# Kernel tuning notes

Hardware: AMD Instinct MI355X
Metric: run time of the kernel (lower is better)

Reference implementation:

```python
import jax, jax.numpy as jnp
import numpy as np

B, D, H, W = 1, 4, 48, 48
C, NH = 256, 8
HD = C // NH
KD, KH, KW = 3, 5, 5
KVOL = KD * KH * KW
SCALE = HD ** -0.5


def _nbhd(L, k):
    """Neighborhood start indices (clamped to stay in-bounds, natten semantics)
    and relative-position-bias indices for one axis."""
    i = jnp.arange(L)
    start = jnp.clip(i - k // 2, 0, L - k)            # [L]
    idx = start[:, None] + jnp.arange(k)[None, :]     # [L,k] absolute neighbor index
    rel = idx - i[:, None] + (k - 1)                  # [L,k] rpb index in [0, 2k-2]
    return idx, rel


def setup_inputs() -> dict:
    key = jax.random.key(0)
    ks = jax.random.split(key, 5)
    s = 0.02
    return {
        "x": jax.random.normal(ks[0], (B, D, H, W, C), jnp.float32),
        "w_qkv": jax.random.normal(ks[1], (C, 3 * C), jnp.float32) * s,
        "b_qkv": jnp.zeros((3 * C,), jnp.float32),
        "rpb": jax.random.normal(ks[2], (NH, 2 * KD - 1, 2 * KH - 1, 2 * KW - 1), jnp.float32) * s,
        "w_proj": jax.random.normal(ks[3], (C, C), jnp.float32) * s,
        "b_proj": jnp.zeros((C,), jnp.float32),
    }


def _nat3d(q, k, v, rpb):
    # q,k,v: [B,NH,D,H,W,HD]; q already scaled
    idxD, relD = _nbhd(D, KD)
    idxH, relH = _nbhd(H, KH)
    idxW, relW = _nbhd(W, KW)
    iD = idxD[:, None, None, :, None, None]
    iH = idxH[None, :, None, None, :, None]
    iW = idxW[None, None, :, None, None, :]
    gk = k[:, :, iD, iH, iW]   # [B,NH,D,H,W,KD,KH,KW,HD]
    gv = v[:, :, iD, iH, iW]
    bias = rpb[:, relD[:, None, None, :, None, None],
                  relH[None, :, None, None, :, None],
                  relW[None, None, :, None, None, :]]  # [NH,D,H,W,KD,KH,KW]
    scores = jnp.einsum("bndyxc,bndyxtuvc->bndyxtuv", q, gk) + bias[None]
    flat = scores.reshape(*scores.shape[:5], KVOL)
    attn = jax.nn.softmax(flat, axis=-1).reshape(scores.shape)
    return jnp.einsum("bndyxtuv,bndyxtuvc->bndyxc", attn, gv)


def reference(x, w_qkv, b_qkv, rpb, w_proj, b_proj):
    qkv = (x @ w_qkv + b_qkv).reshape(B, D, H, W, 3, NH, HD)
    qkv = jnp.transpose(qkv, (4, 0, 5, 1, 2, 3, 6))  # [3,B,NH,D,H,W,HD]
    q, k, v = qkv[0] * SCALE, qkv[1], qkv[2]
    out = _nat3d(q, k, v, rpb)                       # [B,NH,D,H,W,HD]
    out = jnp.transpose(out, (0, 2, 3, 4, 1, 5)).reshape(B, D, H, W, C)
    return out @ w_proj + b_proj
```

## Files before the change

### kernel.cpp

```cpp
#include <hip/hip_runtime.h>

#define QK_SCALE 0.17677669529663687f
#define TOKENS 9216

typedef __attribute__((ext_vector_type(8))) __bf16 bf16x8;
typedef __attribute__((ext_vector_type(8))) unsigned short us8;
typedef __attribute__((ext_vector_type(4))) float f32x4;

static __device__ __forceinline__ unsigned short f2bf(float x) {
    unsigned int u = __float_as_uint(x);
    return (unsigned short)((u + 0x7FFFu + ((u >> 16) & 1u)) >> 16);
}
static __device__ __forceinline__ float bf2f(unsigned short u) {
    return __uint_as_float(((unsigned int)u) << 16);
}
static __device__ __forceinline__ bf16x8 ld_bf8(const unsigned short* p) {
    us8 u = *reinterpret_cast<const us8*>(p);
    return __builtin_bit_cast(bf16x8, u);
}

__global__ __launch_bounds__(256) void conv_prep(
    const float* __restrict__ x, const float* __restrict__ wqkv, const float* __restrict__ wproj,
    const float* __restrict__ rpb,
    unsigned short* __restrict__ xb, unsigned short* __restrict__ wqT,
    unsigned short* __restrict__ wpT, unsigned short* __restrict__ biasT)
{
    int b = blockIdx.x, t = threadIdx.x;
    if (b < 2304) {
        int idx = (b * 256 + t) * 4;
        float4 v = *reinterpret_cast<const float4*>(x + idx);
        ushort4 o;
        o.x = f2bf(v.x); o.y = f2bf(v.y); o.z = f2bf(v.z); o.w = f2bf(v.w);
        *reinterpret_cast<ushort4*>(xb + idx) = o;
    } else if (b < 3072) {
        int e = (b - 2304) * 256 + t;
        int n = e >> 8, k = e & 255;
        wqT[n * 256 + k] = f2bf(wqkv[k * 768 + n]);
    } else if (b < 3328) {
        int e = (b - 3072) * 256 + t;
        int n = e >> 8, k = e & 255;
        wpT[n * 256 + k] = f2bf(wproj[k * 256 + n]);
    } else {
        const int bid = b - 3328;
        const int cls = bid >> 3, h = bid & 7;
        const int d  = cls / 9;
        const int r  = cls % 9;
        const int yc = r / 3, xc = r % 3;
        const int by = (yc == 0) ? 0 : ((yc == 1) ? 5 : 11);
        const int bx = (xc == 0) ? 0 : ((xc == 1) ? 5 : 11);
        const int y0 = by * 4, x0 = bx * 4;
        const int base_d = min(max(d - 1, 0), 1);
        const int base_h = min(max(y0 - 2, 0), 40);
        const int base_w = min(max(x0 - 2, 0), 40);
        const int relD = base_d - d + 2;
        unsigned short* dst = biasT + (size_t)bid * 3072;
        for (int idx = t; idx < 3072; idx += 256) {
            int tok = idx / 192;
            int rem = idx - tok * 192;
            int w = rem / 96; rem -= w * 96;
            int g = rem / 24;
            int j = rem - g * 24;
            int i = j >> 2, rg = j & 3;
            int cand = w * 96 + i * 16 + g * 4 + rg;
            int y = y0 + (tok >> 2), xx = x0 + (tok & 3);
            int sh = min(max(y - 2, 0), 43), sw = min(max(xx - 2, 0), 43);
            int ld = cand >> 6, lh = (cand >> 3) & 7, lw = cand & 7;
            int t0 = lh - (sh - base_h), t1 = lw - (sw - base_w);
            bool valid = ((unsigned)t0 < 5u) && ((unsigned)t1 < 5u);
            unsigned short v = 0xFF80;
            if (valid) {
                int bi = (relD + ld) * 81 + (lh - (y - base_h) + 4) * 9 + (lw - (xx - base_w) + 4);
                v = f2bf(rpb[h * 405 + bi]);
            }
            dst[idx] = v;
        }
    }
}

template<int MF, int NF, int MODE>
__global__ __launch_bounds__(256) void gemm_mfma(
    const unsigned short* __restrict__ A, const unsigned short* __restrict__ BT,
    const float* __restrict__ bias,
    unsigned short* __restrict__ oq, unsigned short* __restrict__ ok,
    unsigned short* __restrict__ ov, float* __restrict__ of)
{
    const int tid = threadIdx.x;
    const int wid = tid >> 6, lane = tid & 63;
    const int wm = wid >> 1, wn = wid & 1;
    const int n15 = lane & 15, g = lane >> 4;
    const int m0 = blockIdx.y * (MF * 32) + wm * (MF * 16);
    const int n0 = blockIdx.x * (NF * 32) + wn * (NF * 16);

    f32x4 acc[MF][NF];
    #pragma unroll
    for (int i = 0; i < MF; i++)
        #pragma unroll
        for (int j = 0; j < NF; j++)
            acc[i][j] = f32x4{0.f, 0.f, 0.f, 0.f};

    #pragma unroll
    for (int ks = 0; ks < 8; ++ks) {
        bf16x8 a[MF], b[NF];
        #pragma unroll
        for (int mt = 0; mt < MF; ++mt)
            a[mt] = ld_bf8(A + (size_t)(m0 + mt * 16 + n15) * 256 + ks * 32 + g * 8);
        #pragma unroll
        for (int nt = 0; nt < NF; ++nt)
            b[nt] = ld_bf8(BT + (size_t)(n0 + nt * 16 + n15) * 256 + ks * 32 + g * 8);
        #pragma unroll
        for (int mt = 0; mt < MF; ++mt)
            #pragma unroll
            for (int nt = 0; nt < NF; ++nt)
                acc[mt][nt] = __builtin_amdgcn_mfma_f32_16x16x32_bf16(b[nt], a[mt], acc[mt][nt], 0, 0, 0);
    }

    #pragma unroll
    for (int mt = 0; mt < MF; ++mt) {
        #pragma unroll
        for (int nt = 0; nt < NF; ++nt) {
            int tok = m0 + mt * 16 + n15;
            int nb  = n0 + nt * 16 + g * 4;
            float4 bv4 = *reinterpret_cast<const float4*>(bias + nb);
            float v0 = acc[mt][nt][0] + bv4.x;
            float v1 = acc[mt][nt][1] + bv4.y;
            float v2 = acc[mt][nt][2] + bv4.z;
            float v3 = acc[mt][nt][3] + bv4.w;
            if (MODE == 0) {
                int part = nb >> 8, c = nb & 255, hh = c >> 5, ch = c & 31;
                unsigned short* dst = (part == 0) ? oq : ((part == 1) ? ok : ov);
                if (part == 0) { v0 *= QK_SCALE; v1 *= QK_SCALE; v2 *= QK_SCALE; v3 *= QK_SCALE; }
                ushort4 o;
                o.x = f2bf(v0); o.y = f2bf(v1); o.z = f2bf(v2); o.w = f2bf(v3);
                *reinterpret_cast<ushort4*>(dst + ((size_t)hh * TOKENS + tok) * 32 + ch) = o;
            } else {
                float4 o = make_float4(v0, v1, v2, v3);
                *reinterpret_cast<float4*>(of + (size_t)tok * 256 + nb) = o;
            }
        }
    }
}

__global__ __launch_bounds__(128) void nat_attn_mfma(
    const unsigned short* __restrict__ qws, const unsigned short* __restrict__ kws,
    const unsigned short* __restrict__ vws, const unsigned short* __restrict__ biasT,
    unsigned short* __restrict__ aout)
{
    __shared__ unsigned short VT[32 * 200];
    __shared__ unsigned short Pl[16 * 200];
    __shared__ float red[2][16];

    const int tid = threadIdx.x;
    const int w = tid >> 6, lane = tid & 63;
    const int n15 = lane & 15, g = lane >> 4;

    int b = blockIdx.x;
    const int h = b & 7; b >>= 3;
    const int bx = b % 12; b /= 12;
    const int by = b % 12;
    const int d  = b / 12;
    const int y0 = by * 4, x0 = bx * 4;
    const int base_d = min(max(d - 1, 0), 1);
    const int base_h = min(max(y0 - 2, 0), 40);
    const int base_w = min(max(x0 - 2, 0), 40);

    const int yc = (by == 0) ? 0 : ((by == 11) ? 2 : 1);
    const int xc = (bx == 0) ? 0 : ((bx == 11) ? 2 : 1);
    const unsigned short* bT = biasT + (size_t)(((d * 9 + yc * 3 + xc) * 8 + h)) * 3072;

    const size_t hoff = (size_t)h * TOKENS * 32;
    const unsigned short* kb = kws + hoff;
    const unsigned short* vb = vws + hoff;
    const unsigned short* qb = qws + hoff;

    for (int id = tid; id < 768; id += 128) {
        int cand = id % 192, chg = id / 192;
        int ld = cand >> 6, lh = (cand >> 3) & 7, lw = cand & 7;
        int gt = (base_d + ld) * 2304 + (base_h + lh) * 48 + (base_w + lw);
        us8 u = *reinterpret_cast<const us8*>(vb + (size_t)gt * 32 + chg * 8);
        #pragma unroll
        for (int e = 0; e < 8; e++) VT[(chg * 8 + e) * 200 + cand] = u[e];
    }

    us8 bl[3];
    {
        const unsigned short* bp = bT + (size_t)(((n15 * 2 + w) * 4 + g) * 24);
        bl[0] = *reinterpret_cast<const us8*>(bp);
        bl[1] = *reinterpret_cast<const us8*>(bp + 8);
        bl[2] = *reinterpret_cast<const us8*>(bp + 16);
    }

    const int gtq = d * 2304 + (y0 + (n15 >> 2)) * 48 + (x0 + (n15 & 3));
    bf16x8 qf = ld_bf8(qb + (size_t)gtq * 32 + g * 8);

    f32x4 sf[6];
    #pragma unroll
    for (int i = 0; i < 6; ++i) {
        int cand = (w * 6 + i) * 16 + n15;
        int ld = cand >> 6, lh = (cand >> 3) & 7, lw = cand & 7;
        int gtc = (base_d + ld) * 2304 + (base_h + lh) * 48 + (base_w + lw);
        bf16x8 kf = ld_bf8(kb + (size_t)gtc * 32 + g * 8);
        sf[i] = __builtin_amdgcn_mfma_f32_16x16x32_bf16(kf, qf, f32x4{0.f, 0.f, 0.f, 0.f}, 0, 0, 0);
    }

    float s24 = 0.f;
    uint2 pq[6];
    #pragma unroll
    for (int i = 0; i < 6; ++i) {
        int j = i * 4;
        float e0 = __expf(sf[i][0] + bf2f(bl[(j + 0) >> 3][(j + 0) & 7]));
        float e1 = __expf(sf[i][1] + bf2f(bl[(j + 1) >> 3][(j + 1) & 7]));
        float e2 = __expf(sf[i][2] + bf2f(bl[(j + 2) >> 3][(j + 2) & 7]));
        float e3 = __expf(sf[i][3] + bf2f(bl[(j + 3) >> 3][(j + 3) & 7]));
        s24 += (e0 + e1) + (e2 + e3);
        pq[i].x = (__float_as_uint(e1) & 0xFFFF0000u) | (__float_as_uint(e0) >> 16);
        pq[i].y = (__float_as_uint(e3) & 0xFFFF0000u) | (__float_as_uint(e2) >> 16);
    }
    s24 += __shfl_xor(s24, 16);
    s24 += __shfl_xor(s24, 32);
    if (g == 0) red[w][n15] = s24;

    #pragma unroll
    for (int i = 0; i < 6; ++i)
        *reinterpret_cast<uint2*>(&Pl[n15 * 200 + w * 96 + i * 16 + g * 4]) = pq[i];
    __syncthreads();

    f32x4 oacc = f32x4{0.f, 0.f, 0.f, 0.f};
    #pragma unroll
    for (int ks = 0; ks < 6; ++ks) {
        bf16x8 vf = ld_bf8(&VT[(w * 16 + n15) * 200 + ks * 32 + g * 8]);
        bf16x8 pa = ld_bf8(&Pl[n15 * 200 + ks * 32 + g * 8]);
        oacc = __builtin_amdgcn_mfma_f32_16x16x32_bf16(vf, pa, oacc, 0, 0, 0);
    }
    {
        float inv = 1.f / (red[0][n15] + red[1][n15]);
        int gtr = d * 2304 + (y0 + (n15 >> 2)) * 48 + (x0 + (n15 & 3));
        ushort4 o;
        o.x = f2bf(oacc[0] * inv);
        o.y = f2bf(oacc[1] * inv);
        o.z = f2bf(oacc[2] * inv);
        o.w = f2bf(oacc[3] * inv);
        *reinterpret_cast<ushort4*>(aout + (size_t)gtr * 256 + h * 32 + w * 16 + g * 4) = o;
    }
}

extern "C" void kernel_launch(void* const* d_in, const int* in_sizes, int n_in,
                              void* d_out, int out_size, void* d_ws, size_t ws_size,
                              hipStream_t stream) {
    const float* x      = (const float*)d_in[0];
    const float* w_qkv  = (const float*)d_in[1];
    const float* b_qkv  = (const float*)d_in[2];
    const float* rpb    = (const float*)d_in[3];
    const float* w_proj = (const float*)d_in[4];
    const float* b_proj = (const float*)d_in[5];
    float* out = (float*)d_out;

    unsigned short* ws = (unsigned short*)d_ws;
    unsigned short* xb    = ws;
    unsigned short* wqT   = ws + (size_t)2359296;
    unsigned short* wpT   = ws + (size_t)2555904;
    unsigned short* qws   = ws + (size_t)2621440;
    unsigned short* kws   = ws + (size_t)4980736;
    unsigned short* vws   = ws + (size_t)7340032;
    unsigned short* aws   = ws + (size_t)9699328;
    unsigned short* biasT = ws + (size_t)12058624;

    conv_prep<<<dim3(3616), 256, 0, stream>>>(x, w_qkv, w_proj, rpb, xb, wqT, wpT, biasT);

    gemm_mfma<4, 4, 0><<<dim3(6, 72), 256, 0, stream>>>(xb, wqT, b_qkv, qws, kws, vws, nullptr);

    nat_attn_mfma<<<dim3(4608), 128, 0, stream>>>(qws, kws, vws, biasT, aws);

    gemm_mfma<2, 2, 1><<<dim3(4, 144), 256, 0, stream>>>(aws, wpT, b_proj, nullptr, nullptr, nullptr, out);
}
```

Baseline: 64.61 us.

## Store V transposed from QKV GEMM and load MFMA fragments directly from global

```diff
diff --git a/kernel.cpp b/kernel.cpp
--- a/kernel.cpp
+++ b/kernel.cpp
@@ -5,6 +5,7 @@
 
 typedef __attribute__((ext_vector_type(8))) __bf16 bf16x8;
 typedef __attribute__((ext_vector_type(8))) unsigned short us8;
+typedef unsigned short us8a4 __attribute__((ext_vector_type(8), aligned(4)));
 typedef __attribute__((ext_vector_type(4))) float f32x4;
 
 static __device__ __forceinline__ unsigned short f2bf(float x) {
@@ -17,6 +18,10 @@
 static __device__ __forceinline__ bf16x8 ld_bf8(const unsigned short* p) {
     us8 u = *reinterpret_cast<const us8*>(p);
     return __builtin_bit_cast(bf16x8, u);
+}
+static __device__ __forceinline__ bf16x8 ld_bf8_a4(const unsigned short* p) {
+    us8a4 u = *reinterpret_cast<const us8a4*>(p);
+    return __builtin_bit_cast(bf16x8, (us8)u);
 }
 
 __global__ __launch_bounds__(256) void conv_prep(
@@ -82,7 +87,7 @@
     const unsigned short* __restrict__ A, const unsigned short* __restrict__ BT,
     const float* __restrict__ bias,
     unsigned short* __restrict__ oq, unsigned short* __restrict__ ok,
-    unsigned short* __restrict__ ov, float* __restrict__ of)
+    unsigned short* __restrict__ ovT, float* __restrict__ of)
 {
     const int tid = threadIdx.x;
     const int wid = tid >> 6, lane = tid & 63;
@@ -127,11 +132,22 @@
             float v3 = acc[mt][nt][3] + bv4.w;
             if (MODE == 0) {
                 int part = nb >> 8, c = nb & 255, hh = c >> 5, ch = c & 31;
-                unsigned short* dst = (part == 0) ? oq : ((part == 1) ? ok : ov);
-                if (part == 0) { v0 *= QK_SCALE; v1 *= QK_SCALE; v2 *= QK_SCALE; v3 *= QK_SCALE; }
-                ushort4 o;
-                o.x = f2bf(v0); o.y = f2bf(v1); o.z = f2bf(v2); o.w = f2bf(v3);
-                *reinterpret_cast<ushort4*>(dst + ((size_t)hh * TOKENS + tok) * 32 + ch) = o;
+                if (part == 2) {
+                    int dd = tok / 2304, rem2 = tok - dd * 2304;
+                    int yy = rem2 / 48, xx2 = rem2 - yy * 48;
+                    unsigned short* dstv = ovT + (size_t)hh * 294912
+                                         + ((size_t)(dd * 48 + yy) * 32) * 48 + xx2;
+                    dstv[(ch + 0) * 48] = f2bf(v0);
+                    dstv[(ch + 1) * 48] = f2bf(v1);
+                    dstv[(ch + 2) * 48] = f2bf(v2);
+                    dstv[(ch + 3) * 48] = f2bf(v3);
+                } else {
+                    unsigned short* dst = (part == 0) ? oq : ok;
+                    if (part == 0) { v0 *= QK_SCALE; v1 *= QK_SCALE; v2 *= QK_SCALE; v3 *= QK_SCALE; }
+                    ushort4 o;
+                    o.x = f2bf(v0); o.y = f2bf(v1); o.z = f2bf(v2); o.w = f2bf(v3);
+                    *reinterpret_cast<ushort4*>(dst + ((size_t)hh * TOKENS + tok) * 32 + ch) = o;
+                }
             } else {
                 float4 o = make_float4(v0, v1, v2, v3);
                 *reinterpret_cast<float4*>(of + (size_t)tok * 256 + nb) = o;
@@ -142,10 +158,9 @@
 
 __global__ __launch_bounds__(128) void nat_attn_mfma(
     const unsigned short* __restrict__ qws, const unsigned short* __restrict__ kws,
-    const unsigned short* __restrict__ vws, const unsigned short* __restrict__ biasT,
+    const unsigned short* __restrict__ vT, const unsigned short* __restrict__ biasT,
     unsigned short* __restrict__ aout)
 {
-    __shared__ unsigned short VT[32 * 200];
     __shared__ unsigned short Pl[16 * 200];
     __shared__ float red[2][16];
 
@@ -169,17 +184,7 @@
 
     const size_t hoff = (size_t)h * TOKENS * 32;
     const unsigned short* kb = kws + hoff;
-    const unsigned short* vb = vws + hoff;
     const unsigned short* qb = qws + hoff;
-
-    for (int id = tid; id < 768; id += 128) {
-        int cand = id % 192, chg = id / 192;
-        int ld = cand >> 6, lh = (cand >> 3) & 7, lw = cand & 7;
-        int gt = (base_d + ld) * 2304 + (base_h + lh) * 48 + (base_w + lw);
-        us8 u = *reinterpret_cast<const us8*>(vb + (size_t)gt * 32 + chg * 8);
-        #pragma unroll
-        for (int e = 0; e < 8; e++) VT[(chg * 8 + e) * 200 + cand] = u[e];
-    }
 
     us8 bl[3];
     {
@@ -200,6 +205,18 @@
         int gtc = (base_d + ld) * 2304 + (base_h + lh) * 48 + (base_w + lw);
         bf16x8 kf = ld_bf8(kb + (size_t)gtc * 32 + g * 8);
         sf[i] = __builtin_amdgcn_mfma_f32_16x16x32_bf16(kf, qf, f32x4{0.f, 0.f, 0.f, 0.f}, 0, 0, 0);
+    }
+
+    bf16x8 vf[6];
+    {
+        const unsigned short* vTb = vT + (size_t)h * 294912;
+        #pragma unroll
+        for (int ks = 0; ks < 6; ++ks) {
+            int run = ks * 4 + g;
+            int ld = run >> 3, lh = run & 7;
+            vf[ks] = ld_bf8_a4(vTb + ((size_t)((base_d + ld) * 48 + (base_h + lh)) * 32
+                                      + w * 16 + n15) * 48 + base_w);
+        }
     }
 
     float s24 = 0.f;
@@ -227,9 +244,8 @@
     f32x4 oacc = f32x4{0.f, 0.f, 0.f, 0.f};
     #pragma unroll
     for (int ks = 0; ks < 6; ++ks) {
-        bf16x8 vf = ld_bf8(&VT[(w * 16 + n15) * 200 + ks * 32 + g * 8]);
         bf16x8 pa = ld_bf8(&Pl[n15 * 200 + ks * 32 + g * 8]);
-        oacc = __builtin_amdgcn_mfma_f32_16x16x32_bf16(vf, pa, oacc, 0, 0, 0);
+        oacc = __builtin_amdgcn_mfma_f32_16x16x32_bf16(vf[ks], pa, oacc, 0, 0, 0);
     }
     {
         float inv = 1.f / (red[0][n15] + red[1][n15]);
@@ -260,15 +276,15 @@
     unsigned short* wpT   = ws + (size_t)2555904;
     unsigned short* qws   = ws + (size_t)2621440;
     unsigned short* kws   = ws + (size_t)4980736;
-    unsigned short* vws   = ws + (size_t)7340032;
+    unsigned short* vT    = ws + (size_t)7340032;
     unsigned short* aws   = ws + (size_t)9699328;
     unsigned short* biasT = ws + (size_t)12058624;
 
     conv_prep<<<dim3(3616), 256, 0, stream>>>(x, w_qkv, w_proj, rpb, xb, wqT, wpT, biasT);
 
-    gemm_mfma<4, 4, 0><<<dim3(6, 72), 256, 0, stream>>>(xb, wqT, b_qkv, qws, kws, vws, nullptr);
-
-    nat_attn_mfma<<<dim3(4608), 128, 0, stream>>>(qws, kws, vws, biasT, aws);
+    gemm_mfma<4, 4, 0><<<dim3(6, 72), 256, 0, stream>>>(xb, wqT, b_qkv, qws, kws, vT, nullptr);
+
+    nat_attn_mfma<<<dim3(4608), 128, 0, stream>>>(qws, kws, vT, biasT, aws);
 
     gemm_mfma<2, 2, 1><<<dim3(4, 144), 256, 0, stream>>>(aws, wpT, b_proj, nullptr, nullptr, nullptr, out);
 }
```

After: 65.24 us. Within noise of the previous version (+1.0%).
